# Kernel optimization log

Measured on AMD Instinct MI355X. Metric: run time of the kernel, lower is better.

The kernel has to match this reference:

```python
import jax, jax.numpy as jnp
import numpy as np

B, T, DIM = 2, 2048, 2048
H, HKV, HD = 16, 4, 128
ROPE_BASE = 10000.0
RMS_EPS = 1.1920929e-07  # torch F.rms_norm default eps = finfo(fp32).eps


def setup_inputs() -> dict:
    key = jax.random.key(0)
    ks = jax.random.split(key, 5)
    s = DIM ** -0.5
    return {
        "x": jax.random.normal(ks[0], (B, T, DIM), jnp.float32),
        "Wq": jax.random.normal(ks[1], (DIM, DIM), jnp.float32) * s,
        "Wk": jax.random.normal(ks[2], (DIM, HKV * HD), jnp.float32) * s,
        "Wv": jax.random.normal(ks[3], (DIM, HKV * HD), jnp.float32) * s,
        "Wo": jax.random.normal(ks[4], (DIM, DIM), jnp.float32) * s,
        "q_gain": jnp.ones((H,), jnp.float32),
    }


def _rms_norm(x):
    return x * jax.lax.rsqrt(jnp.mean(x * x, axis=-1, keepdims=True) + RMS_EPS)


def _rotary(t, hd, base, dtype):
    inv_freq = base ** (-jnp.arange(0, hd, 2, dtype=jnp.float32) / hd)  # [hd/2]
    ang = jnp.arange(t, dtype=jnp.float32)[:, None] * inv_freq[None, :]  # [T, hd/2]
    return jnp.cos(ang).astype(dtype), jnp.sin(ang).astype(dtype)


def _apply_rope(x, cos, sin):
    # x: [B, h, T, D]; cos/sin: [T, D/2] broadcast over batch/heads
    d = x.shape[-1] // 2
    x1, x2 = x[..., :d], x[..., d:]
    return jnp.concatenate([x1 * cos + x2 * sin, -x1 * sin + x2 * cos], axis=-1)


def reference(x, Wq, Wk, Wv, Wo, q_gain):
    Bq, Tq, _ = x.shape
    q = (x @ Wq).reshape(Bq, Tq, H, HD).transpose(0, 2, 1, 3)      # [B,H,T,D]
    k = (x @ Wk).reshape(Bq, Tq, HKV, HD).transpose(0, 2, 1, 3)    # [B,Hkv,T,D]
    v = (x @ Wv).reshape(Bq, Tq, HKV, HD).transpose(0, 2, 1, 3)    # [B,Hkv,T,D]
    q = _rms_norm(q)
    k = _rms_norm(k)
    cos, sin = _rotary(Tq, HD, ROPE_BASE, q.dtype)
    q = _apply_rope(q, cos, sin)
    k = _apply_rope(k, cos, sin)
    q = q * q_gain.astype(q.dtype)[None, :, None, None]
    g = H // HKV
    qg = q.reshape(Bq, HKV, g, Tq, HD)
    # causal GQA SDPA
    scores = jnp.einsum('bkgqd,bkld->bkgql', qg, k) * (HD ** -0.5)
    causal = jnp.tril(jnp.ones((Tq, Tq), bool))
    scores = jnp.where(causal, scores, -jnp.inf)
    p = jax.nn.softmax(scores, axis=-1)
    yg = jnp.einsum('bkgql,bkld->bkgqd', p, v)                      # [B,Hkv,g,T,D]
    # XSA: remove component of each output along the token's own value vector
    vn = v / jnp.clip(jnp.linalg.norm(v, axis=-1, keepdims=True), 1e-12)
    vn = vn[:, :, None]                                             # [B,Hkv,1,T,D]
    proj = jnp.sum(yg * vn, axis=-1, keepdims=True) * vn
    y = (yg - proj).reshape(Bq, H, Tq, HD)
    y = y.transpose(0, 2, 1, 3).reshape(Bq, Tq, DIM)
    return y @ Wo
```

## Files before the change

### kernel.cpp

```cpp
#include <hip/hip_runtime.h>

constexpr int SL  = 2048;
constexpr int NB  = 2;
constexpr int NH  = 16;
constexpr int NKV = 4;
constexpr int HDIM = 128;
constexpr int DM  = 2048;

typedef unsigned short u16;
typedef unsigned int   u32;
typedef short s16x8 __attribute__((ext_vector_type(8)));
typedef float f32x4 __attribute__((ext_vector_type(4)));

__device__ inline u16 f2bf(float x) {
  union { float f; u32 u; } c; c.f = x;
  u32 r = c.u + 0x7fffu + ((c.u >> 16) & 1u);
  return (u16)(r >> 16);
}
__device__ inline float bf2f(u16 h) {
  union { u32 u; float f; } c; c.u = ((u32)h) << 16; return c.f;
}
__device__ inline u32 cvtpk_bf16(float lo, float hi) {
  u32 r;
  asm("v_cvt_pk_bf16_f32 %0, %1, %2" : "=v"(r) : "v"(lo), "v"(hi));
  return r;
}

__device__ inline void gload16(const void* g, void* l) {
  __builtin_amdgcn_global_load_lds((const __attribute__((address_space(1))) void*)g,
                                   (__attribute__((address_space(3))) void*)l, 16, 0, 0);
}

__global__ __launch_bounds__(256) void prep(const float* __restrict__ x,
                                            const float* __restrict__ Wq,
                                            const float* __restrict__ Wk,
                                            const float* __restrict__ Wv,
                                            const float* __restrict__ Wo,
                                            u16* __restrict__ xb,
                                            u16* __restrict__ WT,
                                            u16* __restrict__ WoT) {
  __shared__ float ld[64][65];
  int id = blockIdx.x;
  if (id < 4096) {
    long i = ((long)id * 256 + threadIdx.x) * 8;
    float4 a = *(const float4*)(x + i);
    float4 b = *(const float4*)(x + i + 4);
    uint4 ov;
    ov.x = (u32)f2bf(a.x) | ((u32)f2bf(a.y) << 16);
    ov.y = (u32)f2bf(a.z) | ((u32)f2bf(a.w) << 16);
    ov.z = (u32)f2bf(b.x) | ((u32)f2bf(b.y) << 16);
    ov.w = (u32)f2bf(b.z) | ((u32)f2bf(b.w) << 16);
    *(uint4*)(xb + i) = ov;
    return;
  }
  id -= 4096;
  const float* src; u16* dst; int N; long bx, by;
  const int K = 2048;
  if (id < 1024)      { src = Wq; dst = WT;                         N = 2048; bx = id & 31; by = id >> 5; }
  else if (id < 1280) { int j = id - 1024; src = Wk; dst = WT + (size_t)2048 * 2048; N = 512; bx = j & 7; by = j >> 3; }
  else if (id < 1536) { int j = id - 1280; src = Wv; dst = WT + (size_t)2560 * 2048; N = 512; bx = j & 7; by = j >> 3; }
  else                { int j = id - 1536; src = Wo; dst = WoT;                     N = 2048; bx = j & 31; by = j >> 5; }
  int tid = threadIdx.x;
  long c0 = bx * 64, r0 = by * 64;
#pragma unroll
  for (int i = 0; i < 4; ++i) {
    int e = tid + 256 * i;
    int r = e >> 4, cg = e & 15;
    float4 v = *(const float4*)(src + (r0 + r) * N + c0 + cg * 4);
    ld[r][cg * 4 + 0] = v.x;
    ld[r][cg * 4 + 1] = v.y;
    ld[r][cg * 4 + 2] = v.z;
    ld[r][cg * 4 + 3] = v.w;
  }
  __syncthreads();
#pragma unroll
  for (int i = 0; i < 4; ++i) {
    int e = tid + 256 * i;
    int cg = e & 15, rr = e >> 4;
    ushort4 o;
    o.x = f2bf(ld[cg * 4 + 0][rr]);
    o.y = f2bf(ld[cg * 4 + 1][rr]);
    o.z = f2bf(ld[cg * 4 + 2][rr]);
    o.w = f2bf(ld[cg * 4 + 3][rr]);
    *(ushort4*)(dst + (c0 + rr) * K + r0 + cg * 4) = o;
  }
}

template <int BF16OUT>
__global__ __launch_bounds__(256, 2) void gemm_bt(const u16* __restrict__ A,
                                                  const u16* __restrict__ BT,
                                                  float* __restrict__ Cf,
                                                  u16* __restrict__ Cb,
                                                  int M, int N, int K) {
  __shared__ __align__(16) char As[256 * 128];
  __shared__ __align__(16) char Bs[128 * 128];
  const int tid = threadIdx.x;
  const int lane = tid & 63;
  const int w = tid >> 6;
  const int wm = w >> 1, wn = w & 1;
  const int lr = lane & 15, lg = lane >> 4;
  const long bm = (long)blockIdx.x * 256;
  const long bn = (long)blockIdx.y * 128;

  f32x4 acc[8][4] = {};

  const int nt = K >> 6;
#pragma unroll 1
  for (int ti = 0; ti < nt; ++ti) {
    const int kt0 = ti << 6;
#pragma unroll
    for (int i = 0; i < 8; ++i) {
      int c = tid + 256 * i;
      int row = c >> 3;
      int slot = (c & 7) << 4;
      int gs = slot ^ ((row & 7) << 4);
      gload16(A + (bm + row) * K + kt0 + (gs >> 1), As + c * 16);
    }
#pragma unroll
    for (int i = 0; i < 4; ++i) {
      int c = tid + 256 * i;
      int row = c >> 3;
      int slot = (c & 7) << 4;
      int gs = slot ^ ((row & 7) << 4);
      gload16(BT + (bn + row) * K + kt0 + (gs >> 1), Bs + c * 16);
    }
    __syncthreads();

    __builtin_amdgcn_s_setprio(1);
#pragma unroll
    for (int kk = 0; kk < 2; ++kk) {
      int colB = (kk * 32 + lg * 8) * 2;
      s16x8 af[8], bfv[4];
#pragma unroll
      for (int m = 0; m < 8; ++m) {
        int row = wm * 128 + m * 16 + lr;
        af[m] = *(const s16x8*)(As + row * 128 + (colB ^ ((row & 7) << 4)));
      }
#pragma unroll
      for (int n = 0; n < 4; ++n) {
        int row = wn * 64 + n * 16 + lr;
        bfv[n] = *(const s16x8*)(Bs + row * 128 + (colB ^ ((row & 7) << 4)));
      }
#pragma unroll
      for (int m = 0; m < 8; ++m)
#pragma unroll
        for (int n = 0; n < 4; ++n)
          acc[m][n] = __builtin_amdgcn_mfma_f32_16x16x32_bf16(af[m], bfv[n], acc[m][n], 0, 0, 0);
    }
    __builtin_amdgcn_s_setprio(0);
    __syncthreads();
  }

#pragma unroll
  for (int m = 0; m < 8; ++m)
#pragma unroll
    for (int n = 0; n < 4; ++n) {
      long row = bm + wm * 128 + m * 16 + lg * 4;
      long col = bn + wn * 64 + n * 16 + lr;
#pragma unroll
      for (int r = 0; r < 4; ++r) {
        if (BF16OUT)
          Cb[(row + r) * N + col] = f2bf(acc[m][n][r]);
        else
          Cf[(row + r) * N + col] = acc[m][n][r];
      }
    }
}

__global__ __launch_bounds__(256) void postqkv(const u16* __restrict__ qkv,
                                               const float* __restrict__ qg,
                                               u16* __restrict__ qb, u16* __restrict__ kb,
                                               u16* __restrict__ vt) {
  __shared__ u16 ldt[64][136];
  int id = blockIdx.x;
  int tid = threadIdx.x;
  if (id < 4096) {
    int token = id;
    int b = token >> 11, t = token & (SL - 1);
    int lane = tid & 63, w = tid >> 6;
    const u16* row = qkv + (long)token * 3072;
    float inv = __expf(-(float)lane * (9.210340371976184f / 64.0f));
    float ang = (float)t * inv;
    float c = cosf(ang), s = sinf(ang);
    for (int slot = w; slot < 20; slot += 4) {
      const u16* p = row + slot * 128;
      float v0 = bf2f(p[lane]), v1 = bf2f(p[lane + 64]);
      float ss = v0 * v0 + v1 * v1;
      for (int m = 1; m < 64; m <<= 1) ss += __shfl_xor(ss, m);
      float rms = rsqrtf(ss * (1.0f / 128.0f) + 1.1920929e-07f);
      v0 *= rms; v1 *= rms;
      float o0 =  v0 * c + v1 * s;
      float o1 = -v0 * s + v1 * c;
      u16* dst;
      if (slot < 16) {
        float g = qg[slot] * 0.08838834764831845f * 1.4426950408889634f;
        o0 *= g; o1 *= g;
        dst = qb + ((long)(b * NH + slot) * SL + t) * 128;
      } else {
        dst = kb + ((long)(b * NKV + (slot - 16)) * SL + t) * 128;
      }
      dst[lane] = f2bf(o0);
      dst[lane + 64] = f2bf(o1);
    }
    return;
  }
  int blk = id - 4096;
  int tt = blk & 31, kvb = blk >> 5;
  const u16* src = qkv + (long)(((kvb >> 2) * SL) + tt * 64) * 3072 + 2560 + (kvb & 3) * 128;
#pragma unroll
  for (int i = 0; i < 4; ++i) {
    int e = tid + 256 * i;
    int r = e >> 4, dg = e & 15;
    uint4 v = *(const uint4*)(src + (long)r * 3072 + dg * 8);
    *(uint4*)(&ldt[r][dg * 8]) = v;
  }
  __syncthreads();
  u16* dst = vt + (long)kvb * 128 * SL + tt * 64;
#pragma unroll
  for (int i = 0; i < 8; ++i) {
    int e = tid + 256 * i;
    int rg = e & 15, d = e >> 4;
    ushort4 o;
    o.x = ldt[rg * 4 + 0][d];
    o.y = ldt[rg * 4 + 1][d];
    o.z = ldt[rg * 4 + 2][d];
    o.w = ldt[rg * 4 + 3][d];
    *(ushort4*)(dst + (long)d * SL + rg * 4) = o;
  }
}

__global__ __launch_bounds__(256) void attn(const u16* __restrict__ qb, const u16* __restrict__ kb,
                                            const u16* __restrict__ vt, const float* __restrict__ qg,
                                            const u16* __restrict__ qkvb, u16* __restrict__ yb) {
  __shared__ __align__(16) char Ks[2][64 * 256];
  __shared__ __align__(16) char Vs[2][128 * 128];
  __shared__ __align__(16) char Ps[64 * 128];
  const int tid = threadIdx.x, lane = tid & 63, w = tid >> 6;
  const int pairIdx = blockIdx.x;
  const int bh = blockIdx.y;
  const int b = bh >> 4, h = bh & 15;
  const int kvh = h >> 2;
  const int lr = lane & 15, lg = lane >> 4;

  const float Ms = 16.3223f * fabsf(qg[h]);

  const u16* kbase = kb + (long)(b * NKV + kvh) * SL * 128;
  const u16* vbase = vt + (long)(b * NKV + kvh) * 128 * SL;

#pragma unroll 1
  for (int pass = 0; pass < 2; ++pass) {
    const int qblk = pass ? 31 - pairIdx : pairIdx;
    const int ntile = qblk + 1;

    const u16* qp = qb + ((long)bh * SL + qblk * 64 + w * 16 + lr) * 128;
    s16x8 qf[4];
#pragma unroll
    for (int kk = 0; kk < 4; ++kk) qf[kk] = *(const s16x8*)(qp + kk * 32 + lg * 8);

    f32x4 acc[8] = {};
    float lsum[4] = {0.f, 0.f, 0.f, 0.f};

#pragma unroll
    for (int i = 0; i < 4; ++i) {
      int c = tid + 256 * i;
      int row = c >> 4, slot = (c & 15) << 4;
      gload16(kbase + (long)row * 128 + ((slot ^ ((row & 15) << 4)) >> 1), Ks[0] + c * 16);
    }
#pragma unroll
    for (int i = 0; i < 4; ++i) {
      int c = tid + 256 * i;
      int row = c >> 3, slot = (c & 7) << 4;
      gload16(vbase + (long)row * SL + ((slot ^ ((row & 7) << 4)) >> 1), Vs[0] + c * 16);
    }

#pragma unroll 1
    for (int kt = 0; kt < ntile; ++kt) {
      const int cur = kt & 1;
      if (kt + 1 < ntile) {
        const int nx = cur ^ 1;
#pragma unroll
        for (int i = 0; i < 4; ++i) {
          int c = tid + 256 * i;
          int row = c >> 4, slot = (c & 15) << 4;
          gload16(kbase + (long)((kt + 1) * 64 + row) * 128 + ((slot ^ ((row & 15) << 4)) >> 1),
                  Ks[nx] + c * 16);
        }
#pragma unroll
        for (int i = 0; i < 4; ++i) {
          int c = tid + 256 * i;
          int row = c >> 3, slot = (c & 7) << 4;
          gload16(vbase + (long)row * SL + (kt + 1) * 64 + ((slot ^ ((row & 7) << 4)) >> 1),
                  Vs[nx] + c * 16);
        }
        asm volatile("s_waitcnt vmcnt(8)" ::: "memory");
      } else {
        asm volatile("s_waitcnt vmcnt(0)" ::: "memory");
      }
      __builtin_amdgcn_s_barrier();

      f32x4 sv[4];
      __builtin_amdgcn_s_setprio(1);
#pragma unroll
      for (int n = 0; n < 4; ++n) {
        f32x4 z = {0.f, 0.f, 0.f, 0.f};
#pragma unroll
        for (int kk = 0; kk < 4; ++kk) {
          int row = n * 16 + lr;
          s16x8 kf = *(const s16x8*)(Ks[cur] + row * 256 + (((kk * 32 + lg * 8) * 2) ^ ((row & 15) << 4)));
          z = __builtin_amdgcn_mfma_f32_16x16x32_bf16(qf[kk], kf, z, 0, 0, 0);
        }
        sv[n] = z;
      }
      __builtin_amdgcn_s_setprio(0);

      if (kt == qblk) {
#pragma unroll
        for (int n = 0; n < 4; ++n)
#pragma unroll
          for (int r = 0; r < 4; ++r) {
            int colA = n * 16 + lr;
            int rowA = w * 16 + lg * 4 + r;
            if (colA > rowA) sv[n][r] = -1e30f;
          }
      }
#pragma unroll
      for (int n = 0; n < 4; ++n)
#pragma unroll
        for (int r = 0; r < 4; ++r) {
          float p = __builtin_amdgcn_exp2f(sv[n][r] - Ms);
          sv[n][r] = p;
          lsum[r] += p;
        }
#pragma unroll
      for (int n = 0; n < 4; ++n) {
        u32 pk0 = cvtpk_bf16(sv[n][0], sv[n][1]);
        u32 pk1 = cvtpk_bf16(sv[n][2], sv[n][3]);
        int row = w * 16 + lg * 4;
        int colB = (n * 16 + lr) * 2;
        *(u16*)(Ps + (row + 0) * 128 + (colB ^ (((row + 0) & 7) << 4))) = (u16)pk0;
        *(u16*)(Ps + (row + 1) * 128 + (colB ^ (((row + 1) & 7) << 4))) = (u16)(pk0 >> 16);
        *(u16*)(Ps + (row + 2) * 128 + (colB ^ (((row + 2) & 7) << 4))) = (u16)pk1;
        *(u16*)(Ps + (row + 3) * 128 + (colB ^ (((row + 3) & 7) << 4))) = (u16)(pk1 >> 16);
      }
      __builtin_amdgcn_s_setprio(1);
#pragma unroll
      for (int kk = 0; kk < 2; ++kk) {
        int prow = w * 16 + lr;
        s16x8 pa = *(const s16x8*)(Ps + prow * 128 + (((kk * 32 + lg * 8) * 2) ^ ((prow & 7) << 4)));
#pragma unroll
        for (int n = 0; n < 8; ++n) {
          int vrow = n * 16 + lr;
          s16x8 vf = *(const s16x8*)(Vs[cur] + vrow * 128 + (((kk * 32 + lg * 8) * 2) ^ ((vrow & 7) << 4)));
          acc[n] = __builtin_amdgcn_mfma_f32_16x16x32_bf16(pa, vf, acc[n], 0, 0, 0);
        }
      }
      __builtin_amdgcn_s_setprio(0);
      __builtin_amdgcn_s_barrier();
    }

    float inv_l[4];
#pragma unroll
    for (int r = 0; r < 4; ++r) {
      float v = lsum[r];
      v += __shfl_xor(v, 1);
      v += __shfl_xor(v, 2);
      v += __shfl_xor(v, 4);
      v += __shfl_xor(v, 8);
      inv_l[r] = 1.0f / v;
    }
    const int row0 = qblk * 64 + w * 16 + lg * 4;
    float vv[8][4];
    float ssq[4], dot[4];
#pragma unroll
    for (int r = 0; r < 4; ++r) {
      const u16* pr = qkvb + ((long)(b * SL + row0 + r) * 3072) + 2560 + kvh * 128;
      float sq = 0.f;
#pragma unroll
      for (int n = 0; n < 8; ++n) {
        float t = bf2f(pr[n * 16 + lr]);
        vv[n][r] = t;
        sq += t * t;
      }
      ssq[r] = sq;
    }
#pragma unroll
    for (int r = 0; r < 4; ++r) {
      float sq = ssq[r];
      sq += __shfl_xor(sq, 1);
      sq += __shfl_xor(sq, 2);
      sq += __shfl_xor(sq, 4);
      sq += __shfl_xor(sq, 8);
      ssq[r] = sq;
      float d = 0.f;
#pragma unroll
      for (int n = 0; n < 8; ++n) {
        float yn = acc[n][r] * inv_l[r];
        acc[n][r] = yn;
        d += yn * vv[n][r];
      }
      dot[r] = d;
    }
#pragma unroll
    for (int r = 0; r < 4; ++r) {
      float d = dot[r];
      d += __shfl_xor(d, 1);
      d += __shfl_xor(d, 2);
      d += __shfl_xor(d, 4);
      d += __shfl_xor(d, 8);
      dot[r] = d / fmaxf(ssq[r], 1e-24f);
    }
    u16* yp = yb + ((long)(b * SL + row0)) * DM + h * 128;
#pragma unroll
    for (int n = 0; n < 8; ++n)
#pragma unroll
      for (int r = 0; r < 4; ++r)
        yp[(long)r * DM + n * 16 + lr] = f2bf(acc[n][r] - dot[r] * vv[n][r]);
  }
}

extern "C" void kernel_launch(void* const* d_in, const int* in_sizes, int n_in,
                              void* d_out, int out_size, void* d_ws, size_t ws_size,
                              hipStream_t stream) {
  const float* x  = (const float*)d_in[0];
  const float* Wq = (const float*)d_in[1];
  const float* Wk = (const float*)d_in[2];
  const float* Wv = (const float*)d_in[3];
  const float* Wo = (const float*)d_in[4];
  const float* qg = (const float*)d_in[5];
  float* out = (float*)d_out;

  char* p = (char*)d_ws;
  u16* xb    = (u16*)p;   p += (size_t)4096 * 2048 * 2;
  u16* WT    = (u16*)p;   p += (size_t)3072 * 2048 * 2;
  u16* WoT   = (u16*)p;   p += (size_t)2048 * 2048 * 2;
  u16* qkvb  = (u16*)p;   p += (size_t)4096 * 3072 * 2;
  u16* qbuf  = (u16*)p;   p += (size_t)NB * NH * SL * 128 * 2;
  u16* kbuf  = (u16*)p;   p += (size_t)NB * NKV * SL * 128 * 2;
  u16* vtb   = (u16*)p;   p += (size_t)NB * NKV * 128 * SL * 2;
  u16* yb = xb;

  prep<<<6656, 256, 0, stream>>>(x, Wq, Wk, Wv, Wo, xb, WT, WoT);
  gemm_bt<1><<<dim3(16, 24), 256, 0, stream>>>(xb, WT, nullptr, qkvb, 4096, 3072, 2048);
  postqkv<<<4352, 256, 0, stream>>>(qkvb, qg, qbuf, kbuf, vtb);
  attn<<<dim3(16, 32), 256, 0, stream>>>(qbuf, kbuf, vtb, qg, qkvb, yb);
  gemm_bt<0><<<dim3(16, 16), 256, 0, stream>>>(yb, WoT, out, nullptr, 4096, 2048, 2048);
}
```

Measured before the change: 207.9 us.

## Enlarge attention query tile to 128 rows so each wave handles two 16-row groups

The attention kernel now processes 128 query rows per block, with each wave computing two 16-row query fragments against every loaded K/V tile. The goal is to reuse each K/V tile held in shared memory and each K/V fragment read across twice as many MFMAs, halving K/V global traffic and barrier count per query row. The grid shrinks to 8x32 blocks (256 total), which may underfill the GPU's compute units. Register pressure also doubles for accumulators, which could lower occupancy, and the causal mask now covers two diagonal tiles.

```diff
diff --git a/kernel.cpp b/kernel.cpp
--- a/kernel.cpp
+++ b/kernel.cpp
@@ -234,7 +234,7 @@
                                             const u16* __restrict__ qkvb, u16* __restrict__ yb) {
   __shared__ __align__(16) char Ks[2][64 * 256];
   __shared__ __align__(16) char Vs[2][128 * 128];
-  __shared__ __align__(16) char Ps[64 * 128];
+  __shared__ __align__(16) char Ps[128 * 128];
   const int tid = threadIdx.x, lane = tid & 63, w = tid >> 6;
   const int pairIdx = blockIdx.x;
   const int bh = blockIdx.y;
@@ -249,16 +249,19 @@
 
 #pragma unroll 1
   for (int pass = 0; pass < 2; ++pass) {
-    const int qblk = pass ? 31 - pairIdx : pairIdx;
-    const int ntile = qblk + 1;
-
-    const u16* qp = qb + ((long)bh * SL + qblk * 64 + w * 16 + lr) * 128;
-    s16x8 qf[4];
-#pragma unroll
-    for (int kk = 0; kk < 4; ++kk) qf[kk] = *(const s16x8*)(qp + kk * 32 + lg * 8);
-
-    f32x4 acc[8] = {};
-    float lsum[4] = {0.f, 0.f, 0.f, 0.f};
+    const int qblk = pass ? 15 - pairIdx : pairIdx;
+    const int ntile = 2 * qblk + 2;
+
+    s16x8 qf[2][4];
+#pragma unroll
+    for (int qg2 = 0; qg2 < 2; ++qg2) {
+      const u16* qp = qb + ((long)bh * SL + qblk * 128 + w * 32 + qg2 * 16 + lr) * 128;
+#pragma unroll
+      for (int kk = 0; kk < 4; ++kk) qf[qg2][kk] = *(const s16x8*)(qp + kk * 32 + lg * 8);
+    }
+
+    f32x4 acc[2][8] = {};
+    float lsum[2][4] = {};
 
 #pragma unroll
     for (int i = 0; i < 4; ++i) {
@@ -298,123 +301,136 @@
       }
       __builtin_amdgcn_s_barrier();
 
-      f32x4 sv[4];
+      f32x4 z[2][4] = {};
       __builtin_amdgcn_s_setprio(1);
 #pragma unroll
       for (int n = 0; n < 4; ++n) {
-        f32x4 z = {0.f, 0.f, 0.f, 0.f};
 #pragma unroll
         for (int kk = 0; kk < 4; ++kk) {
           int row = n * 16 + lr;
           s16x8 kf = *(const s16x8*)(Ks[cur] + row * 256 + (((kk * 32 + lg * 8) * 2) ^ ((row & 15) << 4)));
-          z = __builtin_amdgcn_mfma_f32_16x16x32_bf16(qf[kk], kf, z, 0, 0, 0);
-        }
-        sv[n] = z;
+          z[0][n] = __builtin_amdgcn_mfma_f32_16x16x32_bf16(qf[0][kk], kf, z[0][n], 0, 0, 0);
+          z[1][n] = __builtin_amdgcn_mfma_f32_16x16x32_bf16(qf[1][kk], kf, z[1][n], 0, 0, 0);
+        }
       }
       __builtin_amdgcn_s_setprio(0);
 
-      if (kt == qblk) {
+      if (kt >= 2 * qblk) {
+        const int coff = (kt - 2 * qblk) * 64;
+#pragma unroll
+        for (int qg2 = 0; qg2 < 2; ++qg2)
+#pragma unroll
+          for (int n = 0; n < 4; ++n)
+#pragma unroll
+            for (int r = 0; r < 4; ++r) {
+              int lcol = coff + n * 16 + lr;
+              int lrow = w * 32 + qg2 * 16 + lg * 4 + r;
+              if (lcol > lrow) z[qg2][n][r] = -1e30f;
+            }
+      }
+#pragma unroll
+      for (int qg2 = 0; qg2 < 2; ++qg2)
 #pragma unroll
         for (int n = 0; n < 4; ++n)
 #pragma unroll
           for (int r = 0; r < 4; ++r) {
-            int colA = n * 16 + lr;
-            int rowA = w * 16 + lg * 4 + r;
-            if (colA > rowA) sv[n][r] = -1e30f;
+            float p = __builtin_amdgcn_exp2f(z[qg2][n][r] - Ms);
+            z[qg2][n][r] = p;
+            lsum[qg2][r] += p;
           }
-      }
-#pragma unroll
-      for (int n = 0; n < 4; ++n)
-#pragma unroll
-        for (int r = 0; r < 4; ++r) {
-          float p = __builtin_amdgcn_exp2f(sv[n][r] - Ms);
-          sv[n][r] = p;
-          lsum[r] += p;
-        }
-#pragma unroll
-      for (int n = 0; n < 4; ++n) {
-        u32 pk0 = cvtpk_bf16(sv[n][0], sv[n][1]);
-        u32 pk1 = cvtpk_bf16(sv[n][2], sv[n][3]);
-        int row = w * 16 + lg * 4;
-        int colB = (n * 16 + lr) * 2;
-        *(u16*)(Ps + (row + 0) * 128 + (colB ^ (((row + 0) & 7) << 4))) = (u16)pk0;
-        *(u16*)(Ps + (row + 1) * 128 + (colB ^ (((row + 1) & 7) << 4))) = (u16)(pk0 >> 16);
-        *(u16*)(Ps + (row + 2) * 128 + (colB ^ (((row + 2) & 7) << 4))) = (u16)pk1;
-        *(u16*)(Ps + (row + 3) * 128 + (colB ^ (((row + 3) & 7) << 4))) = (u16)(pk1 >> 16);
-      }
+#pragma unroll
+      for (int qg2 = 0; qg2 < 2; ++qg2)
+#pragma unroll
+        for (int n = 0; n < 4; ++n) {
+          u32 pk0 = cvtpk_bf16(z[qg2][n][0], z[qg2][n][1]);
+          u32 pk1 = cvtpk_bf16(z[qg2][n][2], z[qg2][n][3]);
+          int row = w * 32 + qg2 * 16 + lg * 4;
+          int colB = (n * 16 + lr) * 2;
+          *(u16*)(Ps + (row + 0) * 128 + (colB ^ (((row + 0) & 7) << 4))) = (u16)pk0;
+          *(u16*)(Ps + (row + 1) * 128 + (colB ^ (((row + 1) & 7) << 4))) = (u16)(pk0 >> 16);
+          *(u16*)(Ps + (row + 2) * 128 + (colB ^ (((row + 2) & 7) << 4))) = (u16)pk1;
+          *(u16*)(Ps + (row + 3) * 128 + (colB ^ (((row + 3) & 7) << 4))) = (u16)(pk1 >> 16);
+        }
       __builtin_amdgcn_s_setprio(1);
 #pragma unroll
       for (int kk = 0; kk < 2; ++kk) {
-        int prow = w * 16 + lr;
-        s16x8 pa = *(const s16x8*)(Ps + prow * 128 + (((kk * 32 + lg * 8) * 2) ^ ((prow & 7) << 4)));
+        int colB = (kk * 32 + lg * 8) * 2;
+        int prow0 = w * 32 + lr;
+        int prow1 = w * 32 + 16 + lr;
+        s16x8 pa0 = *(const s16x8*)(Ps + prow0 * 128 + (colB ^ ((prow0 & 7) << 4)));
+        s16x8 pa1 = *(const s16x8*)(Ps + prow1 * 128 + (colB ^ ((prow1 & 7) << 4)));
 #pragma unroll
         for (int n = 0; n < 8; ++n) {
           int vrow = n * 16 + lr;
-          s16x8 vf = *(const s16x8*)(Vs[cur] + vrow * 128 + (((kk * 32 + lg * 8) * 2) ^ ((vrow & 7) << 4)));
-          acc[n] = __builtin_amdgcn_mfma_f32_16x16x32_bf16(pa, vf, acc[n], 0, 0, 0);
+          s16x8 vf = *(const s16x8*)(Vs[cur] + vrow * 128 + (colB ^ ((vrow & 7) << 4)));
+          acc[0][n] = __builtin_amdgcn_mfma_f32_16x16x32_bf16(pa0, vf, acc[0][n], 0, 0, 0);
+          acc[1][n] = __builtin_amdgcn_mfma_f32_16x16x32_bf16(pa1, vf, acc[1][n], 0, 0, 0);
         }
       }
       __builtin_amdgcn_s_setprio(0);
       __builtin_amdgcn_s_barrier();
     }
 
-    float inv_l[4];
-#pragma unroll
-    for (int r = 0; r < 4; ++r) {
-      float v = lsum[r];
-      v += __shfl_xor(v, 1);
-      v += __shfl_xor(v, 2);
-      v += __shfl_xor(v, 4);
-      v += __shfl_xor(v, 8);
-      inv_l[r] = 1.0f / v;
-    }
-    const int row0 = qblk * 64 + w * 16 + lg * 4;
-    float vv[8][4];
-    float ssq[4], dot[4];
-#pragma unroll
-    for (int r = 0; r < 4; ++r) {
-      const u16* pr = qkvb + ((long)(b * SL + row0 + r) * 3072) + 2560 + kvh * 128;
-      float sq = 0.f;
-#pragma unroll
-      for (int n = 0; n < 8; ++n) {
-        float t = bf2f(pr[n * 16 + lr]);
-        vv[n][r] = t;
-        sq += t * t;
-      }
-      ssq[r] = sq;
-    }
-#pragma unroll
-    for (int r = 0; r < 4; ++r) {
-      float sq = ssq[r];
-      sq += __shfl_xor(sq, 1);
-      sq += __shfl_xor(sq, 2);
-      sq += __shfl_xor(sq, 4);
-      sq += __shfl_xor(sq, 8);
-      ssq[r] = sq;
-      float d = 0.f;
-#pragma unroll
-      for (int n = 0; n < 8; ++n) {
-        float yn = acc[n][r] * inv_l[r];
-        acc[n][r] = yn;
-        d += yn * vv[n][r];
-      }
-      dot[r] = d;
-    }
-#pragma unroll
-    for (int r = 0; r < 4; ++r) {
-      float d = dot[r];
-      d += __shfl_xor(d, 1);
-      d += __shfl_xor(d, 2);
-      d += __shfl_xor(d, 4);
-      d += __shfl_xor(d, 8);
-      dot[r] = d / fmaxf(ssq[r], 1e-24f);
-    }
-    u16* yp = yb + ((long)(b * SL + row0)) * DM + h * 128;
-#pragma unroll
-    for (int n = 0; n < 8; ++n)
-#pragma unroll
-      for (int r = 0; r < 4; ++r)
-        yp[(long)r * DM + n * 16 + lr] = f2bf(acc[n][r] - dot[r] * vv[n][r]);
+#pragma unroll
+    for (int qg2 = 0; qg2 < 2; ++qg2) {
+      float inv_l[4];
+#pragma unroll
+      for (int r = 0; r < 4; ++r) {
+        float v = lsum[qg2][r];
+        v += __shfl_xor(v, 1);
+        v += __shfl_xor(v, 2);
+        v += __shfl_xor(v, 4);
+        v += __shfl_xor(v, 8);
+        inv_l[r] = 1.0f / v;
+      }
+      const int row0 = qblk * 128 + w * 32 + qg2 * 16 + lg * 4;
+      float vv[8][4];
+      float ssq[4], dot[4];
+#pragma unroll
+      for (int r = 0; r < 4; ++r) {
+        const u16* pr = qkvb + ((long)(b * SL + row0 + r) * 3072) + 2560 + kvh * 128;
+        float sq = 0.f;
+#pragma unroll
+        for (int n = 0; n < 8; ++n) {
+          float t = bf2f(pr[n * 16 + lr]);
+          vv[n][r] = t;
+          sq += t * t;
+        }
+        ssq[r] = sq;
+      }
+#pragma unroll
+      for (int r = 0; r < 4; ++r) {
+        float sq = ssq[r];
+        sq += __shfl_xor(sq, 1);
+        sq += __shfl_xor(sq, 2);
+        sq += __shfl_xor(sq, 4);
+        sq += __shfl_xor(sq, 8);
+        ssq[r] = sq;
+        float d = 0.f;
+#pragma unroll
+        for (int n = 0; n < 8; ++n) {
+          float yn = acc[qg2][n][r] * inv_l[r];
+          acc[qg2][n][r] = yn;
+          d += yn * vv[n][r];
+        }
+        dot[r] = d;
+      }
+#pragma unroll
+      for (int r = 0; r < 4; ++r) {
+        float d = dot[r];
+        d += __shfl_xor(d, 1);
+        d += __shfl_xor(d, 2);
+        d += __shfl_xor(d, 4);
+        d += __shfl_xor(d, 8);
+        dot[r] = d / fmaxf(ssq[r], 1e-24f);
+      }
+      u16* yp = yb + ((long)(b * SL + row0)) * DM + h * 128;
+#pragma unroll
+      for (int n = 0; n < 8; ++n)
+#pragma unroll
+        for (int r = 0; r < 4; ++r)
+          yp[(long)r * DM + n * 16 + lr] = f2bf(acc[qg2][n][r] - dot[r] * vv[n][r]);
+    }
   }
 }
 
@@ -442,6 +458,6 @@
   prep<<<6656, 256, 0, stream>>>(x, Wq, Wk, Wv, Wo, xb, WT, WoT);
   gemm_bt<1><<<dim3(16, 24), 256, 0, stream>>>(xb, WT, nullptr, qkvb, 4096, 3072, 2048);
   postqkv<<<4352, 256, 0, stream>>>(qkvb, qg, qbuf, kbuf, vtb);
-  attn<<<dim3(16, 32), 256, 0, stream>>>(qbuf, kbuf, vtb, qg, qkvb, yb);
+  attn<<<dim3(8, 32), 256, 0, stream>>>(qbuf, kbuf, vtb, qg, qkvb, yb);
   gemm_bt<0><<<dim3(16, 16), 256, 0, stream>>>(yb, WoT, out, nullptr, 4096, 2048, 2048);
 }
```

Result: slower. 223.7 us (+7.6%).

## Add double-buffered 256x256-tile GEMM for the QKV projection

Applied to the files above, without the earlier changes.

Introduces a 512-thread GEMM kernel with 256x256 output tiles and two LDS buffers, prefetching the next K slice with async loads while computing the current one, and interleaving fragment loads with MFMA groups. It replaces the 256x128 tile kernel for the QKV projection to raise data reuse and hide global memory latency. The larger tile halves the block count, risking CU underutilization, and the LDS footprint limits occupancy.

```diff
diff --git a/kernel.cpp b/kernel.cpp
--- a/kernel.cpp
+++ b/kernel.cpp
@@ -2,9 +2,8 @@
 
 constexpr int SL  = 2048;
 constexpr int NB  = 2;
+constexpr int NKV = 4;
 constexpr int NH  = 16;
-constexpr int NKV = 4;
-constexpr int HDIM = 128;
 constexpr int DM  = 2048;
 
 typedef unsigned short u16;
@@ -86,11 +85,136 @@
   }
 }
 
-template <int BF16OUT>
+__global__ __launch_bounds__(512, 2) void gemm256(const u16* __restrict__ A,
+                                                  const u16* __restrict__ BT,
+                                                  u16* __restrict__ Cb,
+                                                  int M, int N, int K) {
+  __shared__ __align__(16) char As[2][256 * 128];
+  __shared__ __align__(16) char Bs[2][256 * 128];
+  const int tid = threadIdx.x;
+  const int lane = tid & 63;
+  const int wid = tid >> 6;
+  const int wm = wid >> 2, wn = wid & 3;
+  const int lr = lane & 15, lg = lane >> 4;
+  const long bm = (long)blockIdx.x * 256;
+  const long bn = (long)blockIdx.y * 256;
+
+  f32x4 acc[8][4] = {};
+
+  auto stage = [&](int kt0, int buf) {
+#pragma unroll
+    for (int i = 0; i < 4; ++i) {
+      int c = tid + 512 * i;
+      int row = c >> 3;
+      int slot = (c & 7) << 4;
+      int gs = slot ^ ((row & 7) << 4);
+      gload16(A + (bm + row) * K + kt0 + (gs >> 1), As[buf] + c * 16);
+    }
+#pragma unroll
+    for (int i = 0; i < 4; ++i) {
+      int c = tid + 512 * i;
+      int row = c >> 3;
+      int slot = (c & 7) << 4;
+      int gs = slot ^ ((row & 7) << 4);
+      gload16(BT + (bn + row) * K + kt0 + (gs >> 1), Bs[buf] + c * 16);
+    }
+  };
+
+  const int nt = K >> 6;
+  stage(0, 0);
+
+#pragma unroll 1
+  for (int ti = 0; ti < nt; ++ti) {
+    const int cur = ti & 1;
+    if (ti + 1 < nt) {
+      stage((ti + 1) << 6, cur ^ 1);
+      asm volatile("s_waitcnt vmcnt(8)" ::: "memory");
+    } else {
+      asm volatile("s_waitcnt vmcnt(0)" ::: "memory");
+    }
+    __builtin_amdgcn_s_barrier();
+
+    __builtin_amdgcn_s_setprio(1);
+    s16x8 bf01[2][2], bf23[2][2], afk[4][2];
+#pragma unroll
+    for (int n = 0; n < 2; ++n)
+#pragma unroll
+      for (int kk = 0; kk < 2; ++kk) {
+        int row = wn * 64 + n * 16 + lr;
+        int colB = (kk * 32 + lg * 8) * 2;
+        bf01[n][kk] = *(const s16x8*)(Bs[cur] + row * 128 + (colB ^ ((row & 7) << 4)));
+      }
+#pragma unroll
+    for (int m = 0; m < 4; ++m)
+#pragma unroll
+      for (int kk = 0; kk < 2; ++kk) {
+        int row = wm * 128 + m * 16 + lr;
+        int colB = (kk * 32 + lg * 8) * 2;
+        afk[m][kk] = *(const s16x8*)(As[cur] + row * 128 + (colB ^ ((row & 7) << 4)));
+      }
+#pragma unroll
+    for (int kk = 0; kk < 2; ++kk)
+#pragma unroll
+      for (int m = 0; m < 4; ++m)
+#pragma unroll
+        for (int n = 0; n < 2; ++n)
+          acc[m][n] = __builtin_amdgcn_mfma_f32_16x16x32_bf16(afk[m][kk], bf01[n][kk], acc[m][n], 0, 0, 0);
+#pragma unroll
+    for (int n = 0; n < 2; ++n)
+#pragma unroll
+      for (int kk = 0; kk < 2; ++kk) {
+        int row = wn * 64 + (n + 2) * 16 + lr;
+        int colB = (kk * 32 + lg * 8) * 2;
+        bf23[n][kk] = *(const s16x8*)(Bs[cur] + row * 128 + (colB ^ ((row & 7) << 4)));
+      }
+#pragma unroll
+    for (int kk = 0; kk < 2; ++kk)
+#pragma unroll
+      for (int m = 0; m < 4; ++m)
+#pragma unroll
+        for (int n = 0; n < 2; ++n)
+          acc[m][n + 2] = __builtin_amdgcn_mfma_f32_16x16x32_bf16(afk[m][kk], bf23[n][kk], acc[m][n + 2], 0, 0, 0);
+#pragma unroll
+    for (int m = 0; m < 4; ++m)
+#pragma unroll
+      for (int kk = 0; kk < 2; ++kk) {
+        int row = wm * 128 + (m + 4) * 16 + lr;
+        int colB = (kk * 32 + lg * 8) * 2;
+        afk[m][kk] = *(const s16x8*)(As[cur] + row * 128 + (colB ^ ((row & 7) << 4)));
+      }
+#pragma unroll
+    for (int kk = 0; kk < 2; ++kk)
+#pragma unroll
+      for (int m = 0; m < 4; ++m)
+#pragma unroll
+        for (int n = 0; n < 2; ++n)
+          acc[m + 4][n] = __builtin_amdgcn_mfma_f32_16x16x32_bf16(afk[m][kk], bf01[n][kk], acc[m + 4][n], 0, 0, 0);
+#pragma unroll
+    for (int kk = 0; kk < 2; ++kk)
+#pragma unroll
+      for (int m = 0; m < 4; ++m)
+#pragma unroll
+        for (int n = 0; n < 2; ++n)
+          acc[m + 4][n + 2] = __builtin_amdgcn_mfma_f32_16x16x32_bf16(afk[m][kk], bf23[n][kk], acc[m + 4][n + 2], 0, 0, 0);
+    __builtin_amdgcn_s_setprio(0);
+    __builtin_amdgcn_s_barrier();
+  }
+
+#pragma unroll
+  for (int m = 0; m < 8; ++m)
+#pragma unroll
+    for (int n = 0; n < 4; ++n) {
+      long row = bm + wm * 128 + m * 16 + lg * 4;
+      long col = bn + wn * 64 + n * 16 + lr;
+#pragma unroll
+      for (int r = 0; r < 4; ++r)
+        Cb[(row + r) * N + col] = f2bf(acc[m][n][r]);
+    }
+}
+
 __global__ __launch_bounds__(256, 2) void gemm_bt(const u16* __restrict__ A,
                                                   const u16* __restrict__ BT,
                                                   float* __restrict__ Cf,
-                                                  u16* __restrict__ Cb,
                                                   int M, int N, int K) {
   __shared__ __align__(16) char As[256 * 128];
   __shared__ __align__(16) char Bs[128 * 128];
@@ -158,12 +282,8 @@
       long row = bm + wm * 128 + m * 16 + lg * 4;
       long col = bn + wn * 64 + n * 16 + lr;
 #pragma unroll
-      for (int r = 0; r < 4; ++r) {
-        if (BF16OUT)
-          Cb[(row + r) * N + col] = f2bf(acc[m][n][r]);
-        else
-          Cf[(row + r) * N + col] = acc[m][n][r];
-      }
+      for (int r = 0; r < 4; ++r)
+        Cf[(row + r) * N + col] = acc[m][n][r];
     }
 }
 
@@ -440,8 +560,8 @@
   u16* yb = xb;
 
   prep<<<6656, 256, 0, stream>>>(x, Wq, Wk, Wv, Wo, xb, WT, WoT);
-  gemm_bt<1><<<dim3(16, 24), 256, 0, stream>>>(xb, WT, nullptr, qkvb, 4096, 3072, 2048);
+  gemm256<<<dim3(16, 12), 512, 0, stream>>>(xb, WT, qkvb, 4096, 3072, 2048);
   postqkv<<<4352, 256, 0, stream>>>(qkvb, qg, qbuf, kbuf, vtb);
   attn<<<dim3(16, 32), 256, 0, stream>>>(qbuf, kbuf, vtb, qg, qkvb, yb);
-  gemm_bt<0><<<dim3(16, 16), 256, 0, stream>>>(yb, WoT, out, nullptr, 4096, 2048, 2048);
-}
+  gemm_bt<<<dim3(16, 16), 256, 0, stream>>>(yb, WoT, out, 4096, 2048, 2048);
+}
```

Result: slower. 214.9 us (+3.3%).
